# Kernel tuning notes

Hardware: AMD Instinct MI355X
Metric: run time of the kernel (lower is better)

Reference implementation:

```python
import jax, jax.numpy as jnp
import numpy as np

REACH = 3  # neighborhood reach -> 24 causal neighbors, 48 MLP input features


def setup_inputs() -> dict:
    key = jax.random.key(0)
    ks = jax.random.split(key, 5)
    b, c, h, w = 8, 3, 192, 192
    x = jax.random.uniform(ks[0], (b, c, h, w), dtype=jnp.float32)

    def lin(k, fi, fo):
        k1, k2 = jax.random.split(k)
        s = 1.0 / np.sqrt(fi).astype(np.float32)
        W = jax.random.uniform(k1, (fi, fo), minval=-s, maxval=s, dtype=jnp.float32)
        bias = jax.random.uniform(k2, (fo,), minval=-s, maxval=s, dtype=jnp.float32)
        return W, bias

    W1, b1 = lin(ks[1], 48, 96)
    W2, b2 = lin(ks[2], 96, 24)
    W3, b3 = lin(ks[3], 24, 12)
    W4, b4 = lin(ks[4], 12, 1)
    return dict(x=x, W1=W1, b1=b1, W2=W2, b2=b2, W3=W3, b3=b3, W4=W4, b4=b4)


def _forward(x, W1, b1, W2, b2, W3, b3, W4, b4):
    b, c, h, w = x.shape
    r = REACH
    H2, Wd = h - 2 * r, w - 2 * r  # interior grid of predicted pixels

    # Precompute the 24 image-neighborhood taps for every interior pixel.
    # Order matches torch get_nb: 3 rows above (7 cols each, row-major), then 3 cols left.
    slabs = [x[:, :, dy:dy + H2, dx:dx + Wd] for dy in range(r) for dx in range(2 * r + 1)]
    slabs += [x[:, :, r:r + H2, dx:dx + Wd] for dx in range(r)]
    xnb = jnp.transpose(jnp.stack(slabs, axis=-1), (2, 3, 0, 1, 4))   # (H2, Wd, b, c, 24)
    xtgt = jnp.transpose(x[:, :, r:r + H2, r:r + Wd], (2, 3, 0, 1))    # (H2, Wd, b, c)

    def mlp(f):  # f: (b, c, 48)
        f = jnp.tanh(f @ W1 + b1)
        f = jnp.tanh(f @ W2 + b2)
        f = jnp.tanh(f @ W3 + b3)
        f = jnp.tanh(f @ W4 + b4)
        return f[..., 0]  # (b, c)

    def row_step(prev3, row_xs):
        # prev3: (b, c, 3, w) = last 3 full (zero-padded) delta rows
        xnb_row, xtgt_row = row_xs  # (Wd, b, c, 24), (Wd, b, c)
        # 21 delta taps from the 3 previous rows, vectorized over columns.
        pslabs = [prev3[:, :, dy, dx:dx + Wd] for dy in range(r) for dx in range(2 * r + 1)]
        pnb = jnp.transpose(jnp.stack(pslabs, axis=-1), (2, 0, 1, 3))  # (Wd, b, c, 21)

        def col_step(last3, xs):
            # last3: (b, c, 3) = 3 most recent deltas in current row (zeros at row start)
            xn, pn, tgt = xs
            feat = jnp.concatenate([xn, pn, last3], axis=-1)  # (b, c, 48)
            delta = tgt - mlp(feat)
            last3 = jnp.concatenate([last3[:, :, 1:], delta[:, :, None]], axis=-1)
            return last3, delta

        last3_0 = jnp.zeros((b, c, r), x.dtype)
        _, row_d = jax.lax.scan(col_step, last3_0, (xnb_row, pnb, xtgt_row))  # (Wd, b, c)
        row_full = jnp.pad(jnp.transpose(row_d, (1, 2, 0)), ((0, 0), (0, 0), (r, w - r - Wd)))
        prev3 = jnp.concatenate([prev3[:, :, 1:, :], row_full[:, :, None, :]], axis=2)
        return prev3, row_d

    prev3_0 = jnp.zeros((b, c, r, w), x.dtype)
    _, all_d = jax.lax.scan(row_step, prev3_0, (xnb, xtgt))  # (H2, Wd, b, c)

    # torch averages square(deltas) over the full (b, c, h-2, w) buffer, whose
    # only nonzeros are the (H2, Wd) interior deltas.
    total = b * c * (h - 2) * w
    return jnp.sqrt(jnp.sum(all_d * all_d) / total)


def reference(x, W1, b1, W2, b2, W3, b3, W4, b4):
    return _forward(x, W1, b1, W2, b2, W3, b3, W4, b4)
```

## Files before the change

kernel.cpp:

```cpp
#include <hip/hip_runtime.h>

#define NPLANES 24
#define IMG 192
#define RW 194
#define GRID2 186
#define NPIX (GRID2 * GRID2)
#define SLACK 4
#define TSTEPS (926 + 11 * SLACK)

typedef _Float16 f16x8 __attribute__((ext_vector_type(8)));
typedef _Float16 h2v   __attribute__((ext_vector_type(2)));
typedef float    f32x4 __attribute__((ext_vector_type(4)));
typedef __fp16   fp16x2 __attribute__((ext_vector_type(2)));

__device__ float PreBuf[(unsigned long long)NPLANES * NPIX * 100];

__device__ __forceinline__ h2v pk(float a, float b) {
  union { fp16x2 p; h2v h; } u;
  u.p = __builtin_amdgcn_cvt_pkrtz(a, b);
  return u.h;
}
__device__ __forceinline__ unsigned pkn(float a, float b) {
  union { _Float16 h[2]; unsigned u; } x;
  x.h[0] = (_Float16)a; x.h[1] = (_Float16)b;
  return x.u;
}
__device__ __forceinline__ float fast_tanh(float x) {
  float e = __builtin_amdgcn_exp2f(x * 2.885390081777927f);
  return __builtin_fmaf(-2.0f, __builtin_amdgcn_rcpf(e + 1.0f), 1.0f);
}
__device__ __forceinline__ f32x4 tanh4(f32x4 x) {
  const float K = 2.885390081777927f;
  const float a0 = __builtin_amdgcn_exp2f(x[0] * K) + 1.0f;
  const float a1 = __builtin_amdgcn_exp2f(x[1] * K) + 1.0f;
  const float a2 = __builtin_amdgcn_exp2f(x[2] * K) + 1.0f;
  const float a3 = __builtin_amdgcn_exp2f(x[3] * K) + 1.0f;
  const float q01 = a0 * a1, q23 = a2 * a3;
  const float r = __builtin_amdgcn_rcpf(q01 * q23);
  const float r01 = r * q23, r23 = r * q01;
  f32x4 o;
  o[0] = __builtin_fmaf(-2.0f, r01 * a1, 1.0f);
  o[1] = __builtin_fmaf(-2.0f, r01 * a0, 1.0f);
  o[2] = __builtin_fmaf(-2.0f, r23 * a3, 1.0f);
  o[3] = __builtin_fmaf(-2.0f, r23 * a2, 1.0f);
  return o;
}

__launch_bounds__(192)
__global__ void prepass_kernel(const float* __restrict__ x,
                               const float* __restrict__ W1g,
                               const float* __restrict__ b1g)
{
  __shared__ float xs[4][IMG];
  const int tid = threadIdx.x;
  const int plane = blockIdx.x / GRID2;
  const int a = blockIdx.x - plane * GRID2;
  const float* __restrict__ xp = x + (size_t)plane * (IMG * IMG) + (size_t)a * IMG;
  #pragma unroll
  for (int r = 0; r < 4; ++r) xs[r][tid] = xp[r * IMG + tid];
  __syncthreads();
  if (tid >= GRID2) return;

  float f[24];
  #pragma unroll
  for (int dy = 0; dy < 3; ++dy)
    #pragma unroll
    for (int dx = 0; dx < 7; ++dx) f[7 * dy + dx] = xs[dy][tid + dx];
  #pragma unroll
  for (int dx = 0; dx < 3; ++dx) f[21 + dx] = xs[3][tid + dx];

  float acc[96];
  #pragma unroll
  for (int n = 0; n < 96; ++n) acc[n] = b1g[n];
  #pragma unroll
  for (int k = 0; k < 24; ++k) {
    const float fk = f[k];
    const float* __restrict__ wr = W1g + k * 96;
    #pragma unroll
    for (int n = 0; n < 96; ++n) acc[n] = fmaf(fk, wr[n], acc[n]);
  }

  float* op = PreBuf + (size_t)(plane * NPIX + a * GRID2 + tid) * 100;
  #pragma unroll
  for (int g = 0; g < 4; ++g)
    #pragma unroll
    for (int nt = 0; nt < 6; ++nt) {
      float4 st;
      st.x = acc[32 * (nt >> 1) + 8 * g + 4 * (nt & 1) + 0];
      st.y = acc[32 * (nt >> 1) + 8 * g + 4 * (nt & 1) + 1];
      st.z = acc[32 * (nt >> 1) + 8 * g + 4 * (nt & 1) + 2];
      st.w = acc[32 * (nt >> 1) + 8 * g + 4 * (nt & 1) + 3];
      *(float4*)(op + g * 24 + nt * 4) = st;
    }
  op[96] = xs[3][tid + 3];
}

__launch_bounds__(192)
__global__ void codec_kernel(const float* __restrict__ x,
                             const float* __restrict__ W1g, const float* __restrict__ b1g,
                             const float* __restrict__ W2g, const float* __restrict__ b2g,
                             const float* __restrict__ W3g, const float* __restrict__ b3g,
                             const float* __restrict__ W4g, const float* __restrict__ b4g,
                             float* __restrict__ ws)
{
  __shared__ __align__(16) _Float16 ringH[64 * RW];
  __shared__ int   ctrL[4];
  __shared__ float wsum[3];

  const int tid  = threadIdx.x;
  const int lane = tid & 63;
  const int w    = __builtin_amdgcn_readfirstlane(tid >> 6);
  const int lam  = lane & 15;
  const int quad = lane >> 4;
  const int cell = 16 * w + lam;
  const float* __restrict__ pre = PreBuf + (size_t)blockIdx.x * NPIX * 100;
  (void)x; (void)b1g;

  { unsigned* z = (unsigned*)ringH; for (int u = tid; u < 64 * RW / 2; u += 192) z[u] = 0; }
  if (tid < 4) ctrL[tid] = -1;

  f16x8 A1s[6];
  #pragma unroll
  for (int nt = 0; nt < 6; ++nt) {
    union { _Float16 h[8]; f16x8 v; } u;
    const int n1 = 32 * (nt >> 1) + 8 * (lam >> 2) + 4 * (nt & 1) + (lam & 3);
    #pragma unroll
    for (int e = 0; e < 8; ++e) {
      float v = 0.f;
      if (quad == 0) {
        if (e < 2) v = W1g[(46 - e) * 96 + n1];
      } else if (quad == 1) {
        if (e < 6) v = W1g[(38 + e) * 96 + n1];
      } else if (e < 7) {
        v = W1g[(24 + 7 * (3 - quad) + e) * 96 + n1];
      }
      u.h[e] = (_Float16)v;
    }
    A1s[nt] = u.v;
  }
  f16x8 A1f[6];
  #pragma unroll
  for (int nt = 0; nt < 6; ++nt) {
    union { _Float16 h[8]; f16x8 v; } u;
    const int n1 = 32 * (nt >> 1) + 8 * (lam >> 2) + 4 * (nt & 1) + (lam & 3);
    #pragma unroll
    for (int e = 0; e < 8; ++e) {
      float v = 0.f;
      if (quad == 0 && e < 2) v = W1g[((e == 0) ? 44 : 47) * 96 + n1];
      u.h[e] = (_Float16)v;
    }
    A1f[nt] = u.v;
  }
  f16x8 A2[2][3];
  #pragma unroll
  for (int mt = 0; mt < 2; ++mt) {
    const int n2 = 8 * (lam >> 2) + 4 * mt + (lam & 3);
    #pragma unroll
    for (int kt = 0; kt < 3; ++kt) {
      union { _Float16 h[8]; f16x8 v; } u;
      #pragma unroll
      for (int e = 0; e < 8; ++e) {
        const int k2 = 32 * kt + 8 * quad + e;
        u.h[e] = (n2 < 24) ? (_Float16)W2g[k2 * 24 + n2] : (_Float16)0.f;
      }
      A2[mt][kt] = u.v;
    }
  }
  f16x8 A3;
  { union { _Float16 h[8]; f16x8 v; } u;
    #pragma unroll
    for (int e = 0; e < 8; ++e) {
      const int k3 = 8 * quad + e;
      u.h[e] = (k3 < 24 && lam < 12) ? (_Float16)W3g[k3 * 12 + lam] : (_Float16)0.f;
    }
    A3 = u.v; }
  f16x8 A4;
  { union { _Float16 h[8]; f16x8 v; } u;
    #pragma unroll
    for (int e = 0; e < 8; ++e) {
      const int m = 4 * quad + e;
      u.h[e] = ((lam & 3) == 0 && e < 4 && m < 12) ? (_Float16)W4g[m] : (_Float16)0.f;
    }
    A4 = u.v; }

  f32x4 b2q[2], b3q, b4q;
  #pragma unroll
  for (int mt = 0; mt < 2; ++mt)
    #pragma unroll
    for (int r = 0; r < 4; ++r) {
      const int n2 = 8 * quad + 4 * mt + r;
      b2q[mt][r] = (n2 < 24) ? b2g[n2] : 0.f;
    }
  #pragma unroll
  for (int r = 0; r < 4; ++r)
    b3q[r] = (4 * quad + r < 12) ? b3g[4 * quad + r] : 0.f;
  { const float b4v = b4g[0]; b4q[0] = b4v; b4q[1] = b4v; b4q[2] = b4v; b4q[3] = b4v; }

  __syncthreads();

  const int prodw = (w == 0) ? 2 : w - 1;
  const unsigned flagRA = (unsigned)(size_t)&ctrL[prodw];
  const unsigned flagWA = (unsigned)(size_t)&ctrL[w];
  const unsigned* ru32 = (const unsigned*)ringH;
  const unsigned short* rhu = (const unsigned short*)ringH;
  int* const prodCtr = &ctrL[prodw];

  int i  = cell;
  int jj = -(4 * cell + SLACK * w);
  unsigned dl1g = 0, dl2g = 0;
  unsigned bfx0 = 0;
  float sumsq = 0.f, xtA = 0.f, xtB = 0.f;
  f32x4 SA[6], SB[6], PreP[6];
  #pragma unroll
  for (int q = 0; q < 6; ++q) {
    SA[q] = (f32x4){0.f,0.f,0.f,0.f};
    SB[q] = (f32x4){0.f,0.f,0.f,0.f};
    PreP[q] = (f32x4){0.f,0.f,0.f,0.f};
  }

  {
    if (jj >= 0 && i <= 185) {
      const float* pp = pre + (size_t)(i * GRID2 + jj) * 100;
      const f32x4* pv = (const f32x4*)(pp + quad * 24);
      #pragma unroll
      for (int q = 0; q < 6; ++q) PreP[q] = pv[q];
      xtA = pp[96];
    }
    const int rq = quad ? quad : 3;
    const int e0 = jj & ~1;
    const int dwi = ((i - rq) & 63) * 97 + (e0 >> 1);
    const unsigned w0 = ru32[dwi], w1 = ru32[dwi + 1];
    const unsigned w2 = ru32[dwi + 2], w3 = ru32[dwi + 3];
    const bool odd = jj & 1;
    const unsigned a01 = (w0 >> 16) | (w1 << 16);
    const unsigned a12 = (w1 >> 16) | (w2 << 16);
    const unsigned a23 = (w2 >> 16) | (w3 << 16);
    const unsigned t0 = odd ? a01 : w0, t1 = odd ? a12 : w1;
    const unsigned t2 = odd ? a23 : w2, t3 = odd ? (w3 >> 16) : w3;
    union { unsigned u[4]; f16x8 v; } bs;
    bs.u[0] = quad ? t0 : 0u;
    bs.u[1] = quad ? t1 : 0u;
    bs.u[2] = quad ? t2 : 0u;
    bs.u[3] = quad ? t3 : 0u;
    #pragma unroll
    for (int nt = 0; nt < 6; ++nt)
      SA[nt] = __builtin_amdgcn_mfma_f32_16x16x32_f16(A1s[nt], bs.v, PreP[nt], 0, 0, 0);
  }

#define SUBSTEP(T, SC, SN, XTC, XTN)                                            \
  {                                                                             \
    int _cv;                                                                    \
    asm volatile("ds_read_b32 %0, %1" : "=v"(_cv) : "v"(flagRA));               \
    const bool _act = (jj >= 0) && (i <= 185);                                  \
    const int _cb = 3 + jj;                                                     \
    int _iN = i, _jN = jj + 1;                                                  \
    if (_jN > 185) { _iN += 48; _jN -= 192 + 3 * SLACK; }                       \
                       \
    const int _rq = quad ? quad : 3;                                            \
    const int _e0 = _jN & ~1;                                                   \
    const int _dwi = ((_iN - _rq) & 63) * 97 + (_e0 >> 1);                      \
    const unsigned _w0 = ru32[_dwi],     _w1 = ru32[_dwi + 1];                  \
    const unsigned _w2 = ru32[_dwi + 2], _w3 = ru32[_dwi + 3];                  \
    const unsigned short _lf = rhu[((_iN - 1) & 63) * RW + (_jN + 6)];          \
    const unsigned _q0d = dl1g | (dl2g << 16);                                  \
    if (_jN >= 0 && _iN <= 185) {                                               \
      const float* _pp = pre + (size_t)(_iN * GRID2 + _jN) * 100;               \
      const f32x4* _pv = (const f32x4*)(_pp + quad * 24);                       \
      PreP[0]=_pv[0]; PreP[1]=_pv[1]; PreP[2]=_pv[2];                           \
      PreP[3]=_pv[3]; PreP[4]=_pv[4]; PreP[5]=_pv[5];                           \
      XTN = _pp[96];                                                            \
    }                                                                           \
                                      \
    union { unsigned u[4]; f16x8 v; } _bfx;                                     \
    _bfx.u[0] = bfx0; _bfx.u[1] = 0u; _bfx.u[2] = 0u; _bfx.u[3] = 0u;           \
    f32x4 _h1a[6];                                                              \
    _Pragma("unroll")                                                           \
    for (int nt = 0; nt < 6; ++nt)                                              \
      _h1a[nt] = __builtin_amdgcn_mfma_f32_16x16x32_f16(A1f[nt], _bfx.v, SC[nt], 0, 0, 0); \
    f16x8 _B2f[3];                                                              \
    _Pragma("unroll")                                                           \
    for (int kt = 0; kt < 3; ++kt) {                                            \
      const f32x4 _ta = tanh4(_h1a[2 * kt]);                                    \
      const f32x4 _tb = tanh4(_h1a[2 * kt + 1]);                                \
      union { h2v p[4]; f16x8 v; } _u;                                          \
      _u.p[0] = pk(_ta[0], _ta[1]);                                             \
      _u.p[1] = pk(_ta[2], _ta[3]);                                             \
      _u.p[2] = pk(_tb[0], _tb[1]);                                             \
      _u.p[3] = pk(_tb[2], _tb[3]);                                             \
      _B2f[kt] = _u.v;                                                          \
    }                                                                           \
    f32x4 _a20 = b2q[0], _a21 = b2q[1];                                         \
    _a20 = __builtin_amdgcn_mfma_f32_16x16x32_f16(A2[0][0], _B2f[0], _a20, 0, 0, 0); \
    _a20 = __builtin_amdgcn_mfma_f32_16x16x32_f16(A2[0][1], _B2f[1], _a20, 0, 0, 0); \
    _a20 = __builtin_amdgcn_mfma_f32_16x16x32_f16(A2[0][2], _B2f[2], _a20, 0, 0, 0); \
    _a21 = __builtin_amdgcn_mfma_f32_16x16x32_f16(A2[1][0], _B2f[0], _a21, 0, 0, 0); \
    _a21 = __builtin_amdgcn_mfma_f32_16x16x32_f16(A2[1][1], _B2f[1], _a21, 0, 0, 0); \
    _a21 = __builtin_amdgcn_mfma_f32_16x16x32_f16(A2[1][2], _B2f[2], _a21, 0, 0, 0); \
    f16x8 _B3f;                                                                 \
    { const f32x4 _ta = tanh4(_a20);                                            \
      const f32x4 _tb = tanh4(_a21);                                            \
      union { h2v p[4]; f16x8 v; } _u;                                          \
      _u.p[0] = pk(_ta[0], _ta[1]);                                             \
      _u.p[1] = pk(_ta[2], _ta[3]);                                             \
      _u.p[2] = pk(_tb[0], _tb[1]);                                             \
      _u.p[3] = pk(_tb[2], _tb[3]);                                             \
      _B3f = _u.v; }                                                            \
    f32x4 _a3 = __builtin_amdgcn_mfma_f32_16x16x32_f16(A3, _B3f, b3q, 0, 0, 0); \
    f16x8 _B4f;                                                                 \
    { const f32x4 _t3 = tanh4(_a3);                                             \
      union { unsigned u[4]; f16x8 v; } _u;                                     \
      _u.u[0] = pkn(0.f, 0.f);                                                  \
      union { h2v p; unsigned s; } _p0, _p1;                                    \
      _p0.p = pk(_t3[0], _t3[1]);                                               \
      _p1.p = pk(_t3[2], _t3[3]);                                               \
      _u.u[0] = _p0.s; _u.u[1] = _p1.s; _u.u[2] = 0u; _u.u[3] = 0u;             \
      _B4f = _u.v; }                                                            \
    const f32x4 _a4 = __builtin_amdgcn_mfma_f32_16x16x32_f16(A4, _B4f, b4q, 0, 0, 0); \
    const float _pred = fast_tanh(_a4[0]);                                      \
    const float _d = XTC - _pred;                                               \
    const float _de = _act ? _d : 0.f;                                          \
    if (quad == 0) sumsq += _de * _de;                                          \
    if (quad == 0 && _act) ringH[(i & 63) * RW + _cb] = (_Float16)_de;          \
             \
    { union { float f; int b; } _dc; _dc.f = _de;                               \
      int _si = __builtin_amdgcn_update_dpp(0, _dc.b, 0x111, 0xF, 0xF, false);  \
      union { int b; float f; } _sc; _sc.b = _si;                               \
      float _fr = _sc.f;                                                        \
      union { unsigned short s; _Float16 h; } _lh; _lh.s = _lf;                 \
      if (lam == 0) _fr = (float)_lh.h;                                         \
      if (_jN + 3 > 185) _fr = 0.f;                                             \
      bfx0 = (quad == 0) ? pkn(_fr, _de) : 0u; }                                \
                                                            \
    { union { _Float16 h; unsigned short s; } _dh; _dh.h = (_Float16)_de;       \
      if (_act) {                                                               \
        if (jj == 185) { dl1g = 0; dl2g = 0; }                                  \
        else { dl2g = dl1g; dl1g = (unsigned)_dh.s; }                           \
      } }                                                                       \
                                            \
    { const bool _odd = _jN & 1;                                                \
      const unsigned _a01 = (_w0 >> 16) | (_w1 << 16);                          \
      const unsigned _a12 = (_w1 >> 16) | (_w2 << 16);                          \
      const unsigned _a23 = (_w2 >> 16) | (_w3 << 16);                          \
      const unsigned _t0 = _odd ? _a01 : _w0, _t1 = _odd ? _a12 : _w1;          \
      const unsigned _t2 = _odd ? _a23 : _w2, _t3 = _odd ? (_w3 >> 16) : _w3;   \
      union { unsigned u[4]; f16x8 v; } _bs;                                    \
      _bs.u[0] = quad ? _t0 : _q0d;                                             \
      _bs.u[1] = quad ? _t1 : 0u;                                               \
      _bs.u[2] = quad ? _t2 : 0u;                                               \
      _bs.u[3] = quad ? _t3 : 0u;                                               \
      _Pragma("unroll")                                                         \
      for (int nt = 0; nt < 6; ++nt)                                            \
        SN[nt] = __builtin_amdgcn_mfma_f32_16x16x32_f16(A1s[nt], _bs.v, PreP[nt], 0, 0, 0); \
    }                                                                           \
     \
    asm volatile("s_waitcnt lgkmcnt(0)" : "+v"(_cv) :: "memory");               \
    if (_cv < (T) - (SLACK - 1)) {                                              \
      int _g = 0;                                                               \
      do { __builtin_amdgcn_s_sleep(2);                                         \
           _cv = __hip_atomic_load(prodCtr, __ATOMIC_ACQUIRE,                   \
                                   __HIP_MEMORY_SCOPE_WORKGROUP);               \
      } while (_cv < (T) - (SLACK - 1) && ++_g < (1 << 22));                    \
    }                                                                           \
    if (lane == 0)                                                              \
      asm volatile("ds_write_b32 %0, %1" :: "v"(flagWA), "v"(T) : "memory");    \
    asm volatile("" ::: "memory");                                              \
    i = _iN; jj = _jN;                                                          \
  }

  for (int t = 0; t < TSTEPS; t += 2) {
    SUBSTEP(t,     SA, SB, xtA, xtB);
    SUBSTEP(t + 1, SB, SA, xtB, xtA);
  }
#undef SUBSTEP

  #pragma unroll
  for (int off = 32; off >= 1; off >>= 1) sumsq += __shfl_down(sumsq, off);
  if (lane == 0) wsum[w] = sumsq;
  __syncthreads();
  if (tid == 0) ws[blockIdx.x] = wsum[0] + wsum[1] + wsum[2];
}

__global__ void finalize_kernel(const float* __restrict__ ws, float* __restrict__ out) {
  if (threadIdx.x == 0) {
    float s = 0.0f;
    #pragma unroll
    for (int p = 0; p < NPLANES; ++p) s += ws[p];
    out[0] = sqrtf(s / 875520.0f);
  }
}

extern "C" void kernel_launch(void* const* d_in, const int* in_sizes, int n_in,
                              void* d_out, int out_size, void* d_ws, size_t ws_size,
                              hipStream_t stream) {
  (void)in_sizes; (void)n_in; (void)out_size; (void)ws_size;
  const float* x  = (const float*)d_in[0];
  const float* W1 = (const float*)d_in[1];
  const float* b1 = (const float*)d_in[2];
  const float* W2 = (const float*)d_in[3];
  const float* b2 = (const float*)d_in[4];
  const float* W3 = (const float*)d_in[5];
  const float* b3 = (const float*)d_in[6];
  const float* W4 = (const float*)d_in[7];
  const float* b4 = (const float*)d_in[8];
  float* ws = (float*)d_ws;

  prepass_kernel<<<NPLANES * GRID2, 192, 0, stream>>>(x, W1, b1);
  codec_kernel<<<NPLANES, 192, 0, stream>>>(x, W1, b1, W2, b2, W3, b3, W4, b4, ws);
  finalize_kernel<<<1, 64, 0, stream>>>(ws, (float*)d_out);
}
```

Before: 1.249 ms.

## Add odd-shifted LDS ring copy to drop unaligned repacking; raise slack, busy-spin

```diff
diff --git a/kernel.cpp b/kernel.cpp
--- a/kernel.cpp
+++ b/kernel.cpp
@@ -5,7 +5,7 @@
 #define RW 194
 #define GRID2 186
 #define NPIX (GRID2 * GRID2)
-#define SLACK 4
+#define SLACK 6
 #define TSTEPS (926 + 11 * SLACK)
 
 typedef _Float16 f16x8 __attribute__((ext_vector_type(8)));
@@ -104,6 +104,7 @@
                              float* __restrict__ ws)
 {
   __shared__ __align__(16) _Float16 ringH[64 * RW];
+  __shared__ __align__(16) _Float16 ringO[64 * RW];
   __shared__ int   ctrL[4];
   __shared__ float wsum[3];
 
@@ -117,6 +118,7 @@
   (void)x; (void)b1g;
 
   { unsigned* z = (unsigned*)ringH; for (int u = tid; u < 64 * RW / 2; u += 192) z[u] = 0; }
+  { unsigned* z = (unsigned*)ringO; for (int u = tid; u < 64 * RW / 2; u += 192) z[u] = 0; }
   if (tid < 4) ctrL[tid] = -1;
 
   f16x8 A1s[6];
@@ -201,7 +203,8 @@
   const int prodw = (w == 0) ? 2 : w - 1;
   const unsigned flagRA = (unsigned)(size_t)&ctrL[prodw];
   const unsigned flagWA = (unsigned)(size_t)&ctrL[w];
-  const unsigned* ru32 = (const unsigned*)ringH;
+  const unsigned* ru32E = (const unsigned*)ringH;
+  const unsigned* ru32O = (const unsigned*)ringO;
   const unsigned short* rhu = (const unsigned short*)ringH;
   int* const prodCtr = &ctrL[prodw];
 
@@ -227,16 +230,10 @@
       xtA = pp[96];
     }
     const int rq = quad ? quad : 3;
-    const int e0 = jj & ~1;
-    const int dwi = ((i - rq) & 63) * 97 + (e0 >> 1);
-    const unsigned w0 = ru32[dwi], w1 = ru32[dwi + 1];
-    const unsigned w2 = ru32[dwi + 2], w3 = ru32[dwi + 3];
-    const bool odd = jj & 1;
-    const unsigned a01 = (w0 >> 16) | (w1 << 16);
-    const unsigned a12 = (w1 >> 16) | (w2 << 16);
-    const unsigned a23 = (w2 >> 16) | (w3 << 16);
-    const unsigned t0 = odd ? a01 : w0, t1 = odd ? a12 : w1;
-    const unsigned t2 = odd ? a23 : w2, t3 = odd ? (w3 >> 16) : w3;
+    const unsigned* rb = (jj & 1) ? ru32O : ru32E;
+    const int dwi = ((i - rq) & 63) * 97 + (jj >> 1);
+    const unsigned t0 = rb[dwi],     t1 = rb[dwi + 1];
+    const unsigned t2 = rb[dwi + 2], t3 = rb[dwi + 3];
     union { unsigned u[4]; f16x8 v; } bs;
     bs.u[0] = quad ? t0 : 0u;
     bs.u[1] = quad ? t1 : 0u;
@@ -255,12 +252,12 @@
     const int _cb = 3 + jj;                                                     \
     int _iN = i, _jN = jj + 1;                                                  \
     if (_jN > 185) { _iN += 48; _jN -= 192 + 3 * SLACK; }                       \
-                       \
+      \
     const int _rq = quad ? quad : 3;                                            \
-    const int _e0 = _jN & ~1;                                                   \
-    const int _dwi = ((_iN - _rq) & 63) * 97 + (_e0 >> 1);                      \
-    const unsigned _w0 = ru32[_dwi],     _w1 = ru32[_dwi + 1];                  \
-    const unsigned _w2 = ru32[_dwi + 2], _w3 = ru32[_dwi + 3];                  \
+    const unsigned* _rb = (_jN & 1) ? ru32O : ru32E;                            \
+    const int _dwi = ((_iN - _rq) & 63) * 97 + (_jN >> 1);                      \
+    const unsigned _w0 = _rb[_dwi],     _w1 = _rb[_dwi + 1];                    \
+    const unsigned _w2 = _rb[_dwi + 2], _w3 = _rb[_dwi + 3];                    \
     const unsigned short _lf = rhu[((_iN - 1) & 63) * RW + (_jN + 6)];          \
     const unsigned _q0d = dl1g | (dl2g << 16);                                  \
     if (_jN >= 0 && _iN <= 185) {                                               \
@@ -309,7 +306,6 @@
     f16x8 _B4f;                                                                 \
     { const f32x4 _t3 = tanh4(_a3);                                             \
       union { unsigned u[4]; f16x8 v; } _u;                                     \
-      _u.u[0] = pkn(0.f, 0.f);                                                  \
       union { h2v p; unsigned s; } _p0, _p1;                                    \
       _p0.p = pk(_t3[0], _t3[1]);                                               \
       _p1.p = pk(_t3[2], _t3[3]);                                               \
@@ -320,7 +316,10 @@
     const float _d = XTC - _pred;                                               \
     const float _de = _act ? _d : 0.f;                                          \
     if (quad == 0) sumsq += _de * _de;                                          \
-    if (quad == 0 && _act) ringH[(i & 63) * RW + _cb] = (_Float16)_de;          \
+    if (quad == 0 && _act) {                                                    \
+      ringH[(i & 63) * RW + _cb] = (_Float16)_de;                               \
+      ringO[(i & 63) * RW + _cb - 1] = (_Float16)_de;                           \
+    }                                                                           \
              \
     { union { float f; int b; } _dc; _dc.f = _de;                               \
       int _si = __builtin_amdgcn_update_dpp(0, _dc.b, 0x111, 0xF, 0xF, false);  \
@@ -336,29 +335,23 @@
         if (jj == 185) { dl1g = 0; dl2g = 0; }                                  \
         else { dl2g = dl1g; dl1g = (unsigned)_dh.s; }                           \
       } }                                                                       \
-                                            \
-    { const bool _odd = _jN & 1;                                                \
-      const unsigned _a01 = (_w0 >> 16) | (_w1 << 16);                          \
-      const unsigned _a12 = (_w1 >> 16) | (_w2 << 16);                          \
-      const unsigned _a23 = (_w2 >> 16) | (_w3 << 16);                          \
-      const unsigned _t0 = _odd ? _a01 : _w0, _t1 = _odd ? _a12 : _w1;          \
-      const unsigned _t2 = _odd ? _a23 : _w2, _t3 = _odd ? (_w3 >> 16) : _w3;   \
-      union { unsigned u[4]; f16x8 v; } _bs;                                    \
-      _bs.u[0] = quad ? _t0 : _q0d;                                             \
-      _bs.u[1] = quad ? _t1 : 0u;                                               \
-      _bs.u[2] = quad ? _t2 : 0u;                                               \
-      _bs.u[3] = quad ? _t3 : 0u;                                               \
+        \
+    { union { unsigned u[4]; f16x8 v; } _bs;                                    \
+      _bs.u[0] = quad ? _w0 : _q0d;                                             \
+      _bs.u[1] = quad ? _w1 : 0u;                                               \
+      _bs.u[2] = quad ? _w2 : 0u;                                               \
+      _bs.u[3] = quad ? _w3 : 0u;                                               \
       _Pragma("unroll")                                                         \
       for (int nt = 0; nt < 6; ++nt)                                            \
         SN[nt] = __builtin_amdgcn_mfma_f32_16x16x32_f16(A1s[nt], _bs.v, PreP[nt], 0, 0, 0); \
     }                                                                           \
-     \
+      \
     asm volatile("s_waitcnt lgkmcnt(0)" : "+v"(_cv) :: "memory");               \
     if (_cv < (T) - (SLACK - 1)) {                                              \
       int _g = 0;                                                               \
-      do { __builtin_amdgcn_s_sleep(2);                                         \
-           _cv = __hip_atomic_load(prodCtr, __ATOMIC_ACQUIRE,                   \
-                                   __HIP_MEMORY_SCOPE_WORKGROUP);               \
+      do {                                                                      \
+        _cv = __hip_atomic_load(prodCtr, __ATOMIC_ACQUIRE,                      \
+                                __HIP_MEMORY_SCOPE_WORKGROUP);                  \
       } while (_cv < (T) - (SLACK - 1) && ++_g < (1 << 22));                    \
     }                                                                           \
     if (lane == 0)                                                              \
```

Result: slower. 1.277 ms (+2.3%).
